# Optimization experiments

Measured on AMD Instinct MI355X. Metric: run time of the kernel, lower is better.

## Reference

```python
import jax, jax.numpy as jnp
import numpy as np

E = 768
H = 12
DK = E // H
B = 4
S = 2048
EPS = 1e-5


def setup_inputs() -> dict:
    key = jax.random.key(0)
    ks = jax.random.split(key, 8)
    # xavier_uniform bound for square [E, E] weight
    bound = float(np.sqrt(6.0 / (E + E)))
    def xavier(k):
        return jax.random.uniform(k, (E, E), jnp.float32, -bound, bound)
    return {
        "query": jax.random.normal(ks[0], (B, S, E), jnp.float32),
        "key": jax.random.normal(ks[1], (B, S, E), jnp.float32),
        "value": jax.random.normal(ks[2], (B, S, E), jnp.float32),
        "enc_attn_mask": jax.random.randint(ks[3], (B, S, S), 0, 2).astype(bool),
        "Wq": xavier(ks[4]),
        "Wk": xavier(ks[5]),
        "Wv": xavier(ks[6]),
        "Wo": xavier(ks[7]),
    }


def reference(query, key, value, enc_attn_mask, Wq, Wk, Wv, Wo):
    b, s, _ = query.shape
    # projections (nn.Linear: y = x @ W.T), split heads -> [b, h, s, dk]
    Q = (query @ Wq.T).reshape(b, s, H, DK).transpose(0, 2, 1, 3)
    K = (key @ Wk.T).reshape(b, s, H, DK).transpose(0, 2, 1, 3)
    V = (value @ Wv.T).reshape(b, s, H, DK).transpose(0, 2, 1, 3)
    # scaled dot-product attention with boolean mask (True -> -1e9)
    scores = jnp.einsum("bhqd,bhkd->bhqk", Q, K) / np.sqrt(DK).astype(np.float32)
    scores = jnp.where(enc_attn_mask[:, None, :, :], jnp.float32(-1e9), scores)
    attn = jax.nn.softmax(scores, axis=-1)
    context = jnp.einsum("bhqk,bhkd->bhqd", attn, V)
    context = context.transpose(0, 2, 1, 3).reshape(b, s, E)
    out = context @ Wo.T + query  # residual
    # fresh nn.LayerNorm(E): weight=1, bias=0, eps=1e-5
    mean = jnp.mean(out, axis=-1, keepdims=True)
    var = jnp.var(out, axis=-1, keepdims=True)
    return (out - mean) * jax.lax.rsqrt(var + EPS)
```

## Files before the change

### kernel.cpp

```cpp
#include <hip/hip_runtime.h>
#include <stdint.h>
#include <stddef.h>

#define HN   12
#define SN   2048
#define EN   768
#define DKN  64
#define BATCH 4
#define MROWS 8192

typedef short bf16x8 __attribute__((ext_vector_type(8)));
typedef float f32x4 __attribute__((ext_vector_type(4)));

__device__ __forceinline__ unsigned short f2bf(float f) {
  union { float f; unsigned u; } x; x.f = f;
  unsigned r = x.u + 0x7fffu + ((x.u >> 16) & 1u);
  return (unsigned short)(r >> 16);
}

#if __has_builtin(__builtin_amdgcn_cvt_pk_bf16_f32)
typedef __bf16 bf16v2 __attribute__((ext_vector_type(2)));
__device__ __forceinline__ unsigned pk_bf16(float a, float b) {
  union { bf16v2 v; unsigned u; } c;
  c.v = __builtin_amdgcn_cvt_pk_bf16_f32(a, b);
  return c.u;
}
#else
__device__ __forceinline__ unsigned pk_bf16(float a, float b) {
  return (unsigned)f2bf(a) | ((unsigned)f2bf(b) << 16);
}
#endif

#define GLD_LDS16(gptr, lptr) \
  __builtin_amdgcn_global_load_lds((const __attribute__((address_space(1))) void*)(gptr), \
                                   (__attribute__((address_space(3))) void*)(lptr), 16, 0, 0)

#define NBIG4 1572864
#define NW4   147456
__global__ __launch_bounds__(256) void cvt_all(const float* __restrict__ q,
                                               const float* __restrict__ k,
                                               const float* __restrict__ v,
                                               const float* __restrict__ wq,
                                               const float* __restrict__ wk,
                                               const float* __restrict__ wv,
                                               const float* __restrict__ wo,
                                               unsigned short* __restrict__ dst) {
  const int i = blockIdx.x * 256 + threadIdx.x;
  const float* src;
  int off;
  if (i < 3 * NBIG4) {
    const int r = i / NBIG4;
    src = (r == 0) ? q : (r == 1) ? k : v;
    off = i - r * NBIG4;
  } else {
    const int j = i - 3 * NBIG4;
    const int r = j / NW4;
    src = (r == 0) ? wq : (r == 1) ? wk : (r == 2) ? wv : wo;
    off = j - r * NW4;
  }
  float4 val = ((const float4*)src)[off];
  ushort4 o;
  o.x = f2bf(val.x); o.y = f2bf(val.y); o.z = f2bf(val.z); o.w = f2bf(val.w);
  ((ushort4*)dst)[i] = o;
}

__global__ __launch_bounds__(256) void mask_pack(const int* __restrict__ mask,
                                                 unsigned long long* __restrict__ out) {
  const int row = (blockIdx.x * 256 + threadIdx.x) >> 6;
  const int lane = threadIdx.x & 63;
  const int* mrow = mask + (size_t)row * SN;
  unsigned long long* orow = out + (size_t)row * 32;
  for (int kt = 0; kt < 32; ++kt) {
    int v = mrow[kt * 64 + lane];
    unsigned long long bm = __ballot(v != 0);
    if (lane == 0) orow[kt] = bm;
  }
}

template <int MODE>
__global__ __launch_bounds__(256) void gemm_proj(const unsigned short* __restrict__ X,
                                                 const unsigned short* __restrict__ W,
                                                 void* __restrict__ out,
                                                 const float* __restrict__ residual,
                                                 float scale) {
  __shared__ unsigned short As[128 * 32];
  __shared__ unsigned short Bs[128 * 32];
  const int tid  = threadIdx.x;
  const int wave = tid >> 6;
  const int lane = tid & 63;
  const int quad = lane >> 4;
  const int l16  = lane & 15;
  const int bm = blockIdx.x;
  const int bn = blockIdx.y;
  const int wm = wave & 1;
  const int wn = wave >> 1;

  f32x4 acc[4][4] = {};

  const int srow = lane >> 2;
  const int schk = lane & 3;

  for (int bk = 0; bk < 24; ++bk) {
    __syncthreads();
#pragma unroll
    for (int r = 0; r < 2; ++r) {
      const int rowblk = r * 64 + wave * 16;
      GLD_LDS16(X + (size_t)(bm * 128 + rowblk + srow) * EN + bk * 32 + schk * 8,
                As + rowblk * 32);
      GLD_LDS16(W + (size_t)(bn * 128 + rowblk + srow) * EN + bk * 32 + schk * 8,
                Bs + rowblk * 32);
    }
    __syncthreads();

    bf16x8 af[4], bfr[4];
#pragma unroll
    for (int mt = 0; mt < 4; ++mt)
      af[mt] = *(const bf16x8*)&As[(wm * 64 + mt * 16 + l16) * 32 + quad * 8];
#pragma unroll
    for (int nt = 0; nt < 4; ++nt)
      bfr[nt] = *(const bf16x8*)&Bs[(wn * 64 + nt * 16 + l16) * 32 + quad * 8];
#pragma unroll
    for (int mt = 0; mt < 4; ++mt)
#pragma unroll
      for (int nt = 0; nt < 4; ++nt)
        acc[mt][nt] = __builtin_amdgcn_mfma_f32_16x16x32_bf16(af[mt], bfr[nt], acc[mt][nt], 0, 0, 0);
  }

  const int m0 = bm * 128 + wm * 64;
  const int n0 = bn * 128 + wn * 64;

  if (MODE == 0) {
    unsigned short* O = (unsigned short*)out;
#pragma unroll
    for (int mt = 0; mt < 4; ++mt) {
#pragma unroll
      for (int nt = 0; nt < 4; ++nt) {
        const int n = n0 + nt * 16 + l16;
        const int h = n >> 6, d = n & 63;
#pragma unroll
        for (int r = 0; r < 4; ++r) {
          const int m = m0 + mt * 16 + quad * 4 + r;
          const int b = m >> 11, s = m & 2047;
          O[((size_t)(b * HN + h) * SN + s) * DKN + d] = f2bf(acc[mt][nt][r] * scale);
        }
      }
    }
  } else if (MODE == 1) {
    unsigned short* O = (unsigned short*)out;
#pragma unroll
    for (int mt = 0; mt < 4; ++mt) {
#pragma unroll
      for (int nt = 0; nt < 4; ++nt) {
        const int n = n0 + nt * 16 + l16;
        const int h = n >> 6, d = n & 63;
        const int m = m0 + mt * 16 + quad * 4;
        const int b = m >> 11, s = m & 2047;
        ushort4 pk;
        pk.x = f2bf(acc[mt][nt][0]);
        pk.y = f2bf(acc[mt][nt][1]);
        pk.z = f2bf(acc[mt][nt][2]);
        pk.w = f2bf(acc[mt][nt][3]);
        *(ushort4*)&O[((size_t)(b * HN + h) * DKN + d) * SN + s] = pk;
      }
    }
  } else {
    float* O = (float*)out;
#pragma unroll
    for (int mt = 0; mt < 4; ++mt) {
#pragma unroll
      for (int nt = 0; nt < 4; ++nt) {
        const int n = n0 + nt * 16 + l16;
#pragma unroll
        for (int r = 0; r < 4; ++r) {
          const int m = m0 + mt * 16 + quad * 4 + r;
          const size_t idx = (size_t)m * EN + n;
          O[idx] = acc[mt][nt][r] + residual[idx];
        }
      }
    }
  }
}

#define C_LOG2E 1.44269504088896f
#define C_BIAS  17.3123405046630f
__global__ __launch_bounds__(256, 6) void attn_kernel(const unsigned short* __restrict__ Q,
                                                      const unsigned short* __restrict__ K,
                                                      const unsigned short* __restrict__ Vt,
                                                      const unsigned long long* __restrict__ Mbits,
                                                      unsigned short* __restrict__ Ctx) {
  __shared__ unsigned short Ks[64 * 64];
  __shared__ unsigned short Vs[64 * 64];
  __shared__ unsigned short Ps[4][16 * 72];

  const int tid  = threadIdx.x;
  const int wave = tid >> 6, lane = tid & 63;
  const int quad = lane >> 4, l16 = lane & 15;
  const int qt = blockIdx.x, bh = blockIdx.y;
  const int b = bh / HN, h = bh - b * HN;

  const unsigned short* Qp = Q + (size_t)bh * SN * DKN;
  const unsigned short* Kp = K + (size_t)bh * SN * DKN;
  const unsigned short* Vp = Vt + (size_t)bh * DKN * SN;
  const unsigned long long* Mb = Mbits + (size_t)b * SN * 32;

  const int srow = lane >> 3;
  const int schk = lane & 7;
  const int swsrc = (schk ^ srow) * 8;
  const int c0 = (quad ^ (l16 & 7)) * 8;
  const int shA = 31 - l16;
  const int shB = 15 - l16;

  bf16x8 aq0, aq1;
  {
    const int R = qt * 64 + wave * 16 + l16;
    aq0 = *(const bf16x8*)(Qp + (size_t)R * DKN + quad * 8);
    aq1 = *(const bf16x8*)(Qp + (size_t)R * DKN + 32 + quad * 8);
  }

  f32x4 o_acc[4] = {};
  f32x4 l_part = {0.f, 0.f, 0.f, 0.f};

  unsigned short* Pw = Ps[wave];
  const int q0 = qt * 64 + wave * 16 + quad * 4;

  for (int kt = 0; kt < 32; ++kt) {
    __syncthreads();
    {
      const int rb0 = wave * 8, rb1 = 32 + wave * 8;
      GLD_LDS16(Kp + (size_t)(kt * 64 + rb0 + srow) * DKN + swsrc, Ks + rb0 * 64);
      GLD_LDS16(Kp + (size_t)(kt * 64 + rb1 + srow) * DKN + swsrc, Ks + rb1 * 64);
      GLD_LDS16(Vp + (size_t)(rb0 + srow) * SN + kt * 64 + swsrc, Vs + rb0 * 64);
      GLD_LDS16(Vp + (size_t)(rb1 + srow) * SN + kt * 64 + swsrc, Vs + rb1 * 64);
    }

    unsigned long long mw[4];
    const unsigned long long* Mq = Mb + (size_t)q0 * 32 + kt;
#pragma unroll
    for (int r = 0; r < 4; ++r) mw[r] = Mq[r * 32];

    __syncthreads();

    bf16x8 bk[4][2];
#pragma unroll
    for (int nt = 0; nt < 4; ++nt) {
      const int base = (nt * 16 + l16) * 64;
      bk[nt][0] = *(const bf16x8*)&Ks[base + c0];
      bk[nt][1] = *(const bf16x8*)&Ks[base + (c0 ^ 32)];
    }

    f32x4 sfr[4];
#pragma unroll
    for (int nt = 0; nt < 4; ++nt) {
      f32x4 c = {};
      c = __builtin_amdgcn_mfma_f32_16x16x32_bf16(aq0, bk[nt][0], c, 0, 0, 0);
      c = __builtin_amdgcn_mfma_f32_16x16x32_bf16(aq1, bk[nt][1], c, 0, 0, 0);
      sfr[nt] = c;
    }

#pragma unroll
    for (int r = 0; r < 4; ++r) {
      const unsigned lo = (unsigned)mw[r];
      const unsigned hi = (unsigned)(mw[r] >> 32);
      float s0 = ((int)(lo << shA) < 0) ? -1e9f : sfr[0][r];
      float s1 = ((int)(lo << shB) < 0) ? -1e9f : sfr[1][r];
      float s2 = ((int)(hi << shA) < 0) ? -1e9f : sfr[2][r];
      float s3 = ((int)(hi << shB) < 0) ? -1e9f : sfr[3][r];
      const float p0 = __builtin_exp2f(__builtin_fmaf(s0, C_LOG2E, -C_BIAS));
      const float p1 = __builtin_exp2f(__builtin_fmaf(s1, C_LOG2E, -C_BIAS));
      const float p2 = __builtin_exp2f(__builtin_fmaf(s2, C_LOG2E, -C_BIAS));
      const float p3 = __builtin_exp2f(__builtin_fmaf(s3, C_LOG2E, -C_BIAS));
      l_part[r] += (p0 + p1) + (p2 + p3);
      const int row = (quad * 4 + r) * 72;
      const unsigned p01 = pk_bf16(p0, p1);
      const unsigned p23 = pk_bf16(p2, p3);
      Pw[row + l16]      = (unsigned short)p01;
      Pw[row + 16 + l16] = (unsigned short)(p01 >> 16);
      Pw[row + 32 + l16] = (unsigned short)p23;
      Pw[row + 48 + l16] = (unsigned short)(p23 >> 16);
    }
    asm volatile("s_waitcnt lgkmcnt(0)" ::: "memory");

    bf16x8 ap0 = *(const bf16x8*)&Pw[l16 * 72 + quad * 8];
    bf16x8 ap1 = *(const bf16x8*)&Pw[l16 * 72 + 32 + quad * 8];
#pragma unroll
    for (int nt = 0; nt < 4; ++nt) {
      const int base = (nt * 16 + l16) * 64;
      bf16x8 bv0 = *(const bf16x8*)&Vs[base + c0];
      bf16x8 bv1 = *(const bf16x8*)&Vs[base + (c0 ^ 32)];
      o_acc[nt] = __builtin_amdgcn_mfma_f32_16x16x32_bf16(ap0, bv0, o_acc[nt], 0, 0, 0);
      o_acc[nt] = __builtin_amdgcn_mfma_f32_16x16x32_bf16(ap1, bv1, o_acc[nt], 0, 0, 0);
    }
  }

#pragma unroll
  for (int off = 1; off < 16; off <<= 1)
#pragma unroll
    for (int r = 0; r < 4; ++r) l_part[r] += __shfl_xor(l_part[r], off, 64);

#pragma unroll
  for (int r = 0; r < 4; ++r) {
    const float inv = 1.0f / l_part[r];
    const int s = q0 + r;
#pragma unroll
    for (int nt = 0; nt < 4; ++nt) {
      const int col = h * 64 + nt * 16 + l16;
      Ctx[(size_t)(b * SN + s) * EN + col] = f2bf(o_acc[nt][r] * inv);
    }
  }
}

__global__ __launch_bounds__(256) void ln_kernel(const float* __restrict__ X,
                                                 float* __restrict__ Y) {
  const int row = blockIdx.x;
  const int t = threadIdx.x;
  const float* xr = X + (size_t)row * EN;
  float v[3];
  float s = 0.f, ss = 0.f;
#pragma unroll
  for (int i = 0; i < 3; ++i) {
    v[i] = xr[t + i * 256];
    s += v[i];
    ss += v[i] * v[i];
  }
#pragma unroll
  for (int off = 1; off < 64; off <<= 1) {
    s += __shfl_xor(s, off, 64);
    ss += __shfl_xor(ss, off, 64);
  }
  __shared__ float ws_s[4], ws_q[4];
  const int wave = t >> 6, lane = t & 63;
  if (lane == 0) { ws_s[wave] = s; ws_q[wave] = ss; }
  __syncthreads();
  s = ws_s[0] + ws_s[1] + ws_s[2] + ws_s[3];
  ss = ws_q[0] + ws_q[1] + ws_q[2] + ws_q[3];
  const float mean = s * (1.0f / EN);
  const float var = ss * (1.0f / EN) - mean * mean;
  const float rstd = rsqrtf(var + 1e-5f);
  float* yr = Y + (size_t)row * EN;
#pragma unroll
  for (int i = 0; i < 3; ++i) yr[t + i * 256] = (v[i] - mean) * rstd;
}

extern "C" void kernel_launch(void* const* d_in, const int* in_sizes, int n_in,
                              void* d_out, int out_size, void* d_ws, size_t ws_size,
                              hipStream_t stream) {
  (void)in_sizes; (void)n_in; (void)out_size; (void)ws_size;
  const float* query = (const float*)d_in[0];
  const float* key_i = (const float*)d_in[1];
  const float* value = (const float*)d_in[2];
  const int*   mask  = (const int*)d_in[3];
  const float* Wq = (const float*)d_in[4];
  const float* Wk = (const float*)d_in[5];
  const float* Wv = (const float*)d_in[6];
  const float* Wo = (const float*)d_in[7];

  const size_t NBIG = (size_t)MROWS * EN;
  const size_t NW   = (size_t)EN * EN;

  unsigned short* Xq16 = (unsigned short*)d_ws;
  unsigned short* Xk16 = Xq16 + NBIG;
  unsigned short* Xv16 = Xk16 + NBIG;
  unsigned short* Wq16 = Xv16 + NBIG;
  unsigned short* Wk16 = Wq16 + NW;
  unsigned short* Wv16 = Wk16 + NW;
  unsigned short* Wo16 = Wv16 + NW;
  unsigned short* Q16  = Wo16 + NW;
  unsigned short* K16  = Q16 + NBIG;
  unsigned short* Vt16 = K16 + NBIG;
  unsigned short* Ctx16 = Vt16 + NBIG;
  float* OutF = (float*)(Ctx16 + NBIG);
  unsigned long long* Mbits = (unsigned long long*)OutF;

  mask_pack<<<MROWS / 4, 256, 0, stream>>>(mask, Mbits);

  const int ncvt = 3 * NBIG4 + 4 * NW4;
  cvt_all<<<ncvt / 256, 256, 0, stream>>>(query, key_i, value, Wq, Wk, Wv, Wo, Xq16);

  dim3 gg(MROWS / 128, EN / 128);
  gemm_proj<0><<<gg, 256, 0, stream>>>(Xq16, Wq16, Q16, nullptr, 0.125f);
  gemm_proj<0><<<gg, 256, 0, stream>>>(Xk16, Wk16, K16, nullptr, 1.0f);
  gemm_proj<1><<<gg, 256, 0, stream>>>(Xv16, Wv16, Vt16, nullptr, 1.0f);

  attn_kernel<<<dim3(SN / 64, BATCH * HN), 256, 0, stream>>>(Q16, K16, Vt16, Mbits, Ctx16);

  gemm_proj<2><<<gg, 256, 0, stream>>>(Ctx16, Wo16, OutF, query, 1.0f);

  ln_kernel<<<MROWS, 256, 0, stream>>>(OutF, (float*)d_out);
}
```

Baseline: 416.8 us.

## Compute transposed scores so attention probabilities stay in registers for PV MFMA

The attention kernel now computes S^T = K·Q^T, with K as the A operand and a permuted K row load order. The MFMA output layout then matches the B-operand layout needed for P·V. This removes the per-tile LDS staging buffer for P, its stores, the lgkmcnt wait and the reloads. The log2(e) factor is folded into the Q projection scale and the constant exp bias is dropped, which removes an FMA per score but relies on scores staying small enough not to overflow exp2. Each lane now loads a single mask word per tile and writes its context output as a vectorized ushort4 store.

```diff
diff --git a/kernel.cpp b/kernel.cpp
--- a/kernel.cpp
+++ b/kernel.cpp
@@ -181,8 +181,6 @@
   }
 }
 
-#define C_LOG2E 1.44269504088896f
-#define C_BIAS  17.3123405046630f
 __global__ __launch_bounds__(256, 6) void attn_kernel(const unsigned short* __restrict__ Q,
                                                       const unsigned short* __restrict__ K,
                                                       const unsigned short* __restrict__ Vt,
@@ -190,7 +188,6 @@
                                                       unsigned short* __restrict__ Ctx) {
   __shared__ unsigned short Ks[64 * 64];
   __shared__ unsigned short Vs[64 * 64];
-  __shared__ unsigned short Ps[4][16 * 72];
 
   const int tid  = threadIdx.x;
   const int wave = tid >> 6, lane = tid & 63;
@@ -201,111 +198,97 @@
   const unsigned short* Qp = Q + (size_t)bh * SN * DKN;
   const unsigned short* Kp = K + (size_t)bh * SN * DKN;
   const unsigned short* Vp = Vt + (size_t)bh * DKN * SN;
-  const unsigned long long* Mb = Mbits + (size_t)b * SN * 32;
 
   const int srow = lane >> 3;
   const int schk = lane & 7;
   const int swsrc = (schk ^ srow) * 8;
   const int c0 = (quad ^ (l16 & 7)) * 8;
-  const int shA = 31 - l16;
-  const int shB = 15 - l16;
-
-  bf16x8 aq0, aq1;
-  {
-    const int R = qt * 64 + wave * 16 + l16;
-    aq0 = *(const bf16x8*)(Qp + (size_t)R * DKN + quad * 8);
-    aq1 = *(const bf16x8*)(Qp + (size_t)R * DKN + 32 + quad * 8);
-  }
+  const int quad4 = quad * 4;
+
+  const int y0 = wave * 8 + srow;
+  const int y1 = 32 + wave * 8 + srow;
+  const int px0 = (y0 & 32) + (((y0 & 15) >> 2) << 3) + ((y0 >> 4) & 1) * 4 + (y0 & 3);
+  const int px1 = (y1 & 32) + (((y1 & 15) >> 2) << 3) + ((y1 >> 4) & 1) * 4 + (y1 & 3);
+
+  const int R = qt * 64 + wave * 16 + l16;
+  const bf16x8 bq0 = *(const bf16x8*)(Qp + (size_t)R * DKN + quad * 8);
+  const bf16x8 bq1 = *(const bf16x8*)(Qp + (size_t)R * DKN + 32 + quad * 8);
+  const unsigned long long* Mrow = Mbits + ((size_t)(b * SN + R)) * 32;
 
   f32x4 o_acc[4] = {};
-  f32x4 l_part = {0.f, 0.f, 0.f, 0.f};
-
-  unsigned short* Pw = Ps[wave];
-  const int q0 = qt * 64 + wave * 16 + quad * 4;
+  float l_loc = 0.0f;
+  const int shq = 31 - quad * 8;
 
   for (int kt = 0; kt < 32; ++kt) {
     __syncthreads();
     {
       const int rb0 = wave * 8, rb1 = 32 + wave * 8;
-      GLD_LDS16(Kp + (size_t)(kt * 64 + rb0 + srow) * DKN + swsrc, Ks + rb0 * 64);
-      GLD_LDS16(Kp + (size_t)(kt * 64 + rb1 + srow) * DKN + swsrc, Ks + rb1 * 64);
+      GLD_LDS16(Kp + (size_t)(kt * 64 + px0) * DKN + swsrc, Ks + rb0 * 64);
+      GLD_LDS16(Kp + (size_t)(kt * 64 + px1) * DKN + swsrc, Ks + rb1 * 64);
       GLD_LDS16(Vp + (size_t)(rb0 + srow) * SN + kt * 64 + swsrc, Vs + rb0 * 64);
       GLD_LDS16(Vp + (size_t)(rb1 + srow) * SN + kt * 64 + swsrc, Vs + rb1 * 64);
     }
-
-    unsigned long long mw[4];
-    const unsigned long long* Mq = Mb + (size_t)q0 * 32 + kt;
-#pragma unroll
-    for (int r = 0; r < 4; ++r) mw[r] = Mq[r * 32];
-
+    const unsigned long long mw = Mrow[kt];
     __syncthreads();
 
-    bf16x8 bk[4][2];
-#pragma unroll
-    for (int nt = 0; nt < 4; ++nt) {
-      const int base = (nt * 16 + l16) * 64;
-      bk[nt][0] = *(const bf16x8*)&Ks[base + c0];
-      bk[nt][1] = *(const bf16x8*)&Ks[base + (c0 ^ 32)];
-    }
-
-    f32x4 sfr[4];
-#pragma unroll
-    for (int nt = 0; nt < 4; ++nt) {
+    f32x4 st[4];
+#pragma unroll
+    for (int mt = 0; mt < 4; ++mt) {
+      const int base = (mt * 16 + l16) * 64;
+      const bf16x8 ak0 = *(const bf16x8*)&Ks[base + c0];
+      const bf16x8 ak1 = *(const bf16x8*)&Ks[base + (c0 ^ 32)];
       f32x4 c = {};
-      c = __builtin_amdgcn_mfma_f32_16x16x32_bf16(aq0, bk[nt][0], c, 0, 0, 0);
-      c = __builtin_amdgcn_mfma_f32_16x16x32_bf16(aq1, bk[nt][1], c, 0, 0, 0);
-      sfr[nt] = c;
-    }
-
-#pragma unroll
-    for (int r = 0; r < 4; ++r) {
-      const unsigned lo = (unsigned)mw[r];
-      const unsigned hi = (unsigned)(mw[r] >> 32);
-      float s0 = ((int)(lo << shA) < 0) ? -1e9f : sfr[0][r];
-      float s1 = ((int)(lo << shB) < 0) ? -1e9f : sfr[1][r];
-      float s2 = ((int)(hi << shA) < 0) ? -1e9f : sfr[2][r];
-      float s3 = ((int)(hi << shB) < 0) ? -1e9f : sfr[3][r];
-      const float p0 = __builtin_exp2f(__builtin_fmaf(s0, C_LOG2E, -C_BIAS));
-      const float p1 = __builtin_exp2f(__builtin_fmaf(s1, C_LOG2E, -C_BIAS));
-      const float p2 = __builtin_exp2f(__builtin_fmaf(s2, C_LOG2E, -C_BIAS));
-      const float p3 = __builtin_exp2f(__builtin_fmaf(s3, C_LOG2E, -C_BIAS));
-      l_part[r] += (p0 + p1) + (p2 + p3);
-      const int row = (quad * 4 + r) * 72;
-      const unsigned p01 = pk_bf16(p0, p1);
-      const unsigned p23 = pk_bf16(p2, p3);
-      Pw[row + l16]      = (unsigned short)p01;
-      Pw[row + 16 + l16] = (unsigned short)(p01 >> 16);
-      Pw[row + 32 + l16] = (unsigned short)p23;
-      Pw[row + 48 + l16] = (unsigned short)(p23 >> 16);
-    }
-    asm volatile("s_waitcnt lgkmcnt(0)" ::: "memory");
-
-    bf16x8 ap0 = *(const bf16x8*)&Pw[l16 * 72 + quad * 8];
-    bf16x8 ap1 = *(const bf16x8*)&Pw[l16 * 72 + 32 + quad * 8];
-#pragma unroll
-    for (int nt = 0; nt < 4; ++nt) {
-      const int base = (nt * 16 + l16) * 64;
-      bf16x8 bv0 = *(const bf16x8*)&Vs[base + c0];
-      bf16x8 bv1 = *(const bf16x8*)&Vs[base + (c0 ^ 32)];
-      o_acc[nt] = __builtin_amdgcn_mfma_f32_16x16x32_bf16(ap0, bv0, o_acc[nt], 0, 0, 0);
-      o_acc[nt] = __builtin_amdgcn_mfma_f32_16x16x32_bf16(ap1, bv1, o_acc[nt], 0, 0, 0);
-    }
-  }
-
-#pragma unroll
-  for (int off = 1; off < 16; off <<= 1)
-#pragma unroll
-    for (int r = 0; r < 4; ++r) l_part[r] += __shfl_xor(l_part[r], off, 64);
-
-#pragma unroll
-  for (int r = 0; r < 4; ++r) {
-    const float inv = 1.0f / l_part[r];
-    const int s = q0 + r;
-#pragma unroll
-    for (int nt = 0; nt < 4; ++nt) {
-      const int col = h * 64 + nt * 16 + l16;
-      Ctx[(size_t)(b * SN + s) * EN + col] = f2bf(o_acc[nt][r] * inv);
-    }
+      c = __builtin_amdgcn_mfma_f32_16x16x32_bf16(ak0, bq0, c, 0, 0, 0);
+      c = __builtin_amdgcn_mfma_f32_16x16x32_bf16(ak1, bq1, c, 0, 0, 0);
+      st[mt] = c;
+    }
+
+    const unsigned lo = (unsigned)mw;
+    const unsigned hi = (unsigned)(mw >> 32);
+    bf16x8 bp[2];
+#pragma unroll
+    for (int g = 0; g < 2; ++g) {
+      const unsigned w = g ? hi : lo;
+      float p[8];
+#pragma unroll
+      for (int t = 0; t < 2; ++t)
+#pragma unroll
+        for (int r = 0; r < 4; ++r) {
+          const float sv = ((int)(w << (shq - t * 4 - r)) < 0) ? -1e9f : st[g * 2 + t][r];
+          p[t * 4 + r] = __builtin_exp2f(sv);
+        }
+      l_loc += ((p[0] + p[1]) + (p[2] + p[3])) + ((p[4] + p[5]) + (p[6] + p[7]));
+      union { unsigned u[4]; bf16x8 v; } pk;
+      pk.u[0] = pk_bf16(p[0], p[1]);
+      pk.u[1] = pk_bf16(p[2], p[3]);
+      pk.u[2] = pk_bf16(p[4], p[5]);
+      pk.u[3] = pk_bf16(p[6], p[7]);
+      bp[g] = pk.v;
+    }
+
+#pragma unroll
+    for (int dt = 0; dt < 4; ++dt) {
+      const int base = (dt * 16 + l16) * 64;
+      const bf16x8 av0 = *(const bf16x8*)&Vs[base + c0];
+      const bf16x8 av1 = *(const bf16x8*)&Vs[base + (c0 ^ 32)];
+      o_acc[dt] = __builtin_amdgcn_mfma_f32_16x16x32_bf16(av0, bp[0], o_acc[dt], 0, 0, 0);
+      o_acc[dt] = __builtin_amdgcn_mfma_f32_16x16x32_bf16(av1, bp[1], o_acc[dt], 0, 0, 0);
+    }
+  }
+
+  l_loc += __shfl_xor(l_loc, 16, 64);
+  l_loc += __shfl_xor(l_loc, 32, 64);
+  const float inv = 1.0f / l_loc;
+
+  unsigned short* Crow = Ctx + (size_t)(b * SN + R) * EN + h * 64;
+#pragma unroll
+  for (int dt = 0; dt < 4; ++dt) {
+    ushort4 w;
+    w.x = f2bf(o_acc[dt][0] * inv);
+    w.y = f2bf(o_acc[dt][1] * inv);
+    w.z = f2bf(o_acc[dt][2] * inv);
+    w.w = f2bf(o_acc[dt][3] * inv);
+    *(ushort4*)&Crow[dt * 16 + quad4] = w;
   }
 }
 
@@ -377,7 +360,7 @@
   cvt_all<<<ncvt / 256, 256, 0, stream>>>(query, key_i, value, Wq, Wk, Wv, Wo, Xq16);
 
   dim3 gg(MROWS / 128, EN / 128);
-  gemm_proj<0><<<gg, 256, 0, stream>>>(Xq16, Wq16, Q16, nullptr, 0.125f);
+  gemm_proj<0><<<gg, 256, 0, stream>>>(Xq16, Wq16, Q16, nullptr, 0.125f * 1.44269504088896f);
   gemm_proj<0><<<gg, 256, 0, stream>>>(Xk16, Wk16, K16, nullptr, 1.0f);
   gemm_proj<1><<<gg, 256, 0, stream>>>(Xv16, Wv16, Vt16, nullptr, 1.0f);
 
```

New measurement: 383.4 us. 1.09x faster.
